# Performance work log

Measured on AMD Instinct MI355X. Metric: run time of the kernel, lower is better.

The kernel has to match this reference:

```python
import jax, jax.numpy as jnp
import numpy as np

N_EMBD = 1024
N_HEAD = 16
B, T = 4, 2048


def setup_inputs() -> dict:
    key = jax.random.key(0)
    ks = jax.random.split(key, 4)
    s = 1.0 / np.sqrt(N_EMBD)
    return {
        "x": jax.random.normal(ks[0], (B, T, N_EMBD), dtype=jnp.float32),
        "w_attn": jax.random.normal(ks[1], (N_EMBD, 3 * N_EMBD), dtype=jnp.float32) * s,
        "b_attn": jnp.zeros((3 * N_EMBD,), dtype=jnp.float32),
        "w_proj": jax.random.normal(ks[2], (N_EMBD, N_EMBD), dtype=jnp.float32) * s,
        "b_proj": jnp.zeros((N_EMBD,), dtype=jnp.float32),
    }


def reference(x, w_attn, b_attn, w_proj, b_proj):
    Bb, Tt, C = x.shape
    H = N_HEAD
    D = C // H  # head dim
    qkv = x @ w_attn + b_attn  # [B,T,3C]
    q, k, v = jnp.split(qkv, 3, axis=2)
    # [B,H,T,D]
    q = q.reshape(Bb, Tt, H, D).transpose(0, 2, 1, 3)
    k = k.reshape(Bb, Tt, H, D).transpose(0, 2, 1, 3)
    v = v.reshape(Bb, Tt, H, D).transpose(0, 2, 1, 3)
    scale = 1.0 / np.sqrt(D).astype(np.float32)
    attn = jnp.einsum("bhqd,bhkd->bhqk", q, k) * scale
    mask = jnp.tril(jnp.ones((Tt, Tt), dtype=bool))
    attn = jnp.where(mask, attn, jnp.float32(-jnp.inf))
    probs = jax.nn.softmax(attn, axis=-1)
    out = jnp.einsum("bhqk,bhkd->bhqd", probs, v)
    out = out.transpose(0, 2, 1, 3).reshape(Bb, Tt, C)
    return out @ w_proj + b_proj
```

## Files before the change

kernel.cpp:

```cpp
#include <hip/hip_runtime.h>
#include <hip/hip_bf16.h>


typedef float f32x4 __attribute__((ext_vector_type(4)));
typedef short short8 __attribute__((ext_vector_type(8)));
typedef short short4v __attribute__((ext_vector_type(4)));

__device__ __forceinline__ short f2bf(float f) {
  union { __hip_bfloat16 h; short s; } u;
  u.h = __float2bfloat16(f);
  return u.s;
}

__device__ __forceinline__ void gl_lds16(const void* g, void* l) {
  __builtin_amdgcn_global_load_lds(
      (const __attribute__((address_space(1))) void*)g,
      (__attribute__((address_space(3))) void*)l, 16, 0, 0);
}


__global__ void cvt_f32_bf16(const float* __restrict__ in, short* __restrict__ out) {
  int i = (blockIdx.x * 256 + threadIdx.x) * 4;
  float4 v = *(const float4*)(in + i);
  short4v o;
  o[0] = f2bf(v.x); o[1] = f2bf(v.y); o[2] = f2bf(v.z); o[3] = f2bf(v.w);
  *(short4v*)(out + i) = o;
}

__global__ void transpose_cvt(const float* __restrict__ in, short* __restrict__ out,
                              int K, int N) {
  __shared__ float tile[32][33];
  int bx = blockIdx.x * 32;
  int by = blockIdx.y * 32;
  int tx = threadIdx.x, ty = threadIdx.y;
#pragma unroll
  for (int i = 0; i < 32; i += 8)
    tile[ty + i][tx] = in[(size_t)(by + ty + i) * N + bx + tx];
  __syncthreads();
#pragma unroll
  for (int i = 0; i < 32; i += 8)
    out[(size_t)(bx + ty + i) * K + by + tx] = f2bf(tile[tx][ty + i]);
}


#define GEMM_BODY(A_, Bt_)                                                        \
  __shared__ __align__(16) short As[128 * 32];                                    \
  __shared__ __align__(16) short Bs[128 * 32];                                    \
  const int tid = threadIdx.x;                                                    \
  const int wv = tid >> 6;                                                        \
  const int wr = wv >> 1, wc = wv & 1;                                            \
  const int ln = tid & 15, quad = (tid & 63) >> 4;                                \
  const int m0 = blockIdx.y * 128, n0 = blockIdx.x * 128;                         \
  f32x4 acc[4][4];                                                                \
  _Pragma("unroll") for (int i = 0; i < 4; ++i)                                   \
      _Pragma("unroll") for (int j = 0; j < 4; ++j)                               \
          acc[i][j] = (f32x4){0.f, 0.f, 0.f, 0.f};                                \
  for (int k0 = 0; k0 < 1024; k0 += 32) {                                         \
    _Pragma("unroll") for (int i = 0; i < 2; ++i) {                               \
      int cc = tid + i * 256;                                                     \
      int row = cc >> 2, part = cc & 3;                                           \
      gl_lds16(A_ + (size_t)(m0 + row) * 1024 + k0 + part * 8,                    \
               (char*)As + (wv * 64 + i * 256) * 16);                             \
      gl_lds16(Bt_ + (size_t)(n0 + row) * 1024 + k0 + part * 8,                   \
               (char*)Bs + (wv * 64 + i * 256) * 16);                             \
    }                                                                             \
    __syncthreads();                                                              \
    short8 af[4], bf[4];                                                          \
    _Pragma("unroll") for (int i = 0; i < 4; ++i)                                 \
        af[i] = *(const short8*)&As[(wr * 64 + i * 16 + ln) * 32 + quad * 8];     \
    _Pragma("unroll") for (int j = 0; j < 4; ++j)                                 \
        bf[j] = *(const short8*)&Bs[(wc * 64 + j * 16 + ln) * 32 + quad * 8];     \
    _Pragma("unroll") for (int i = 0; i < 4; ++i)                                 \
        _Pragma("unroll") for (int j = 0; j < 4; ++j)                             \
            acc[i][j] =                                                           \
                __builtin_amdgcn_mfma_f32_16x16x32_bf16(af[i], bf[j], acc[i][j],  \
                                                        0, 0, 0);                 \
    __syncthreads();                                                              \
  }

__global__ __launch_bounds__(256, 2) void gemm_qkv(
    const short* __restrict__ A, const short* __restrict__ Bt,
    const float* __restrict__ bias, short* __restrict__ Qb,
    short* __restrict__ Kb, short* __restrict__ Vtb) {
  GEMM_BODY(A, Bt)
#pragma unroll
  for (int i = 0; i < 4; ++i) {
#pragma unroll
    for (int j = 0; j < 4; ++j) {
      int n = n0 + wc * 64 + j * 16 + ln;
      int n2 = n & 1023;
      int hh = n2 >> 6, d = n2 & 63;
      float bv = bias[n];
#pragma unroll
      for (int r = 0; r < 4; ++r) {
        int m = m0 + wr * 64 + i * 16 + quad * 4 + r;
        int bb = m >> 11, t = m & 2047;
        float o = acc[i][j][r] + bv;
        int bh = (bb << 4) + hh;
        if (n < 1024)
          Qb[((size_t)bh * 2048 + t) * 64 + d] = f2bf(o * 0.18033688f);
        else if (n < 2048)
          Kb[((size_t)bh * 2048 + t) * 64 + d] = f2bf(o);
        else
          Vtb[((size_t)bh * 64 + d) * 2048 + t] = f2bf(o);
      }
    }
  }
}

__global__ __launch_bounds__(256, 2) void gemm_proj(
    const short* __restrict__ A, const short* __restrict__ Bt,
    const float* __restrict__ bias, float* __restrict__ out) {
  GEMM_BODY(A, Bt)
#pragma unroll
  for (int i = 0; i < 4; ++i) {
#pragma unroll
    for (int j = 0; j < 4; ++j) {
      int n = n0 + wc * 64 + j * 16 + ln;
      float bv = bias[n];
#pragma unroll
      for (int r = 0; r < 4; ++r) {
        int m = m0 + wr * 64 + i * 16 + quad * 4 + r;
        out[(size_t)m * 1024 + n] = acc[i][j][r] + bv;
      }
    }
  }
}

__global__ __launch_bounds__(256, 3) void flash_attn(
    const short* __restrict__ Qg_, const short* __restrict__ Kg_,
    const short* __restrict__ Vg_, short* __restrict__ Ob) {
  constexpr int STR = 72;
  __shared__ __align__(16) short Kl[64 * STR];
  __shared__ __align__(16) short Vl[64 * STR];
  const int tid = threadIdx.x;
  const int wv = tid >> 6, ln = tid & 15, quad = (tid & 63) >> 4;
  const int q0 = (gridDim.x - 1 - blockIdx.x) * 128;
  const int bh = blockIdx.y;
  const short* Qg = Qg_ + (size_t)bh * 2048 * 64;
  const short* Kg = Kg_ + (size_t)bh * 2048 * 64;
  const short* Vg = Vg_ + (size_t)bh * 64 * 2048;
  const int qbase = q0 + wv * 32;

  short8 qf[2][2];
#pragma unroll
  for (int h = 0; h < 2; ++h)
#pragma unroll
    for (int ch = 0; ch < 2; ++ch)
      qf[h][ch] = *(const short8*)(Qg + (size_t)(qbase + h * 16 + ln) * 64 +
                                   ch * 32 + quad * 8);

  f32x4 Oacc[2][4];
#pragma unroll
  for (int h = 0; h < 2; ++h)
#pragma unroll
    for (int mt = 0; mt < 4; ++mt) Oacc[h][mt] = (f32x4){0.f, 0.f, 0.f, 0.f};
  float lpart[2] = {0.f, 0.f};

  const int ktmax = (q0 + 127) >> 6;
  short8 kreg[2], vreg[2];
  const int srow = tid >> 3, spart = tid & 7;

#define LOADKV(KT)                                                              \
  {                                                                             \
    const short* Kt = Kg + (size_t)(KT) * 64 * 64;                              \
    _Pragma("unroll") for (int i = 0; i < 2; ++i) {                             \
      kreg[i] = *(const short8*)(Kt + (size_t)(srow + i * 32) * 64 + spart * 8);\
      vreg[i] = *(const short8*)(Vg + (size_t)(srow + i * 32) * 2048 +          \
                                 (KT) * 64 + spart * 8);                        \
    }                                                                           \
  }

  LOADKV(0)
  for (int kt = 0; kt <= ktmax; ++kt) {
    __syncthreads();
#pragma unroll
    for (int i = 0; i < 2; ++i) {
      *(short8*)&Kl[(srow + i * 32) * STR + spart * 8] = kreg[i];
      *(short8*)&Vl[(srow + i * 32) * STR + spart * 8] = vreg[i];
    }
    __syncthreads();
    if (kt < ktmax) LOADKV(kt + 1)

    if (kt * 64 <= qbase + 31) {
      f32x4 St[2][4];
#pragma unroll
      for (int h = 0; h < 2; ++h)
#pragma unroll
        for (int kb = 0; kb < 4; ++kb) St[h][kb] = (f32x4){0.f, 0.f, 0.f, 0.f};
#pragma unroll
      for (int kb = 0; kb < 4; ++kb) {
        short8 ka0 = *(const short8*)&Kl[(kb * 16 + ln) * STR + quad * 8];
        short8 ka1 = *(const short8*)&Kl[(kb * 16 + ln) * STR + 32 + quad * 8];
#pragma unroll
        for (int h = 0; h < 2; ++h) {
          St[h][kb] = __builtin_amdgcn_mfma_f32_16x16x32_bf16(ka0, qf[h][0],
                                                              St[h][kb], 0, 0, 0);
          St[h][kb] = __builtin_amdgcn_mfma_f32_16x16x32_bf16(ka1, qf[h][1],
                                                              St[h][kb], 0, 0, 0);
        }
      }

      short4v pf[2][4];
#pragma unroll
      for (int h = 0; h < 2; ++h) {
        const bool needmask = kt * 64 + 63 > qbase + h * 16;
        const int qg = qbase + h * 16 + ln;
#pragma unroll
        for (int kb = 0; kb < 4; ++kb)
#pragma unroll
          for (int r = 0; r < 4; ++r) {
            float s = St[h][kb][r];
            if (needmask) {
              int key = kt * 64 + kb * 16 + quad * 4 + r;
              s = (key <= qg) ? s : -1e30f;
            }
            float p = __builtin_amdgcn_exp2f(s);
            lpart[h] += p;
            union { float f; unsigned u; } c;
            c.f = p;
            pf[h][kb][r] = (short)((c.u + 0x8000u) >> 16);
          }
      }

#pragma unroll
      for (int kb = 0; kb < 4; ++kb)
#pragma unroll
        for (int mt = 0; mt < 4; ++mt) {
          short4v va =
              *(const short4v*)&Vl[(mt * 16 + ln) * STR + kb * 16 + quad * 4];
#pragma unroll
          for (int h = 0; h < 2; ++h)
            Oacc[h][mt] = __builtin_amdgcn_mfma_f32_16x16x16bf16_1k(
                va, pf[h][kb], Oacc[h][mt], 0, 0, 0);
        }
    }
  }

  const int bb = bh >> 4, hh = bh & 15;
#pragma unroll
  for (int h = 0; h < 2; ++h) {
    float l = lpart[h];
    l += __shfl_xor(l, 16);
    l += __shfl_xor(l, 32);
    float rl = 1.0f / l;
    int t = qbase + h * 16 + ln;
#pragma unroll
    for (int mt = 0; mt < 4; ++mt) {
      short4v o;
#pragma unroll
      for (int r = 0; r < 4; ++r) o[r] = f2bf(Oacc[h][mt][r] * rl);
      *(short4v*)(Ob + ((size_t)(bb * 2048 + t)) * 1024 + hh * 64 + mt * 16 +
                  quad * 4) = o;
    }
  }
}


extern "C" void kernel_launch(void* const* d_in, const int* in_sizes, int n_in,
                              void* d_out, int out_size, void* d_ws, size_t ws_size,
                              hipStream_t stream) {
  const float* x      = (const float*)d_in[0];
  const float* w_attn = (const float*)d_in[1];
  const float* b_attn = (const float*)d_in[2];
  const float* w_proj = (const float*)d_in[3];
  const float* b_proj = (const float*)d_in[4];
  float* out = (float*)d_out;
  char* ws = (char*)d_ws;

  short* xb  = (short*)(ws);
  short* wat = (short*)(ws + 16777216);
  short* wpt = (short*)(ws + 23068672);
  short* Qb  = (short*)(ws + 25165824);
  short* Kb  = (short*)(ws + 41943040);
  short* Vtb = (short*)(ws + 58720256);
  short* Ob  = (short*)(ws + 75497472);

  cvt_f32_bf16<<<8192, 256, 0, stream>>>(x, xb);
  transpose_cvt<<<dim3(96, 32), dim3(32, 8), 0, stream>>>(w_attn, wat, 1024, 3072);
  transpose_cvt<<<dim3(32, 32), dim3(32, 8), 0, stream>>>(w_proj, wpt, 1024, 1024);
  gemm_qkv<<<dim3(24, 64), 256, 0, stream>>>(xb, wat, b_attn, Qb, Kb, Vtb);
  flash_attn<<<dim3(16, 64), 256, 0, stream>>>(Qb, Kb, Vtb, Ob);
  gemm_proj<<<dim3(8, 64), 256, 0, stream>>>(Ob, wpt, b_proj, out);
}
```

Measured before the change: 315.4 us.

## Double-buffer K/V in flash attention, pair causal tiles per block, transpose V separately

Flash attention now uses double-buffered LDS for K/V tiles, so each iteration needs one barrier instead of two. Each block handles a complementary pair of query tiles (long and short) to balance causal work across 512 blocks. The QKV GEMM writes V in row layout, which should make its stores coalesced, and a separate transpose kernel builds V^T, reusing the O buffer as scratch. The cost is an extra kernel launch plus a V round-trip through memory, and occupancy drops from 3 to 2 blocks per CU because of the larger LDS footprint.

```diff
diff --git a/kernel.cpp b/kernel.cpp
--- a/kernel.cpp
+++ b/kernel.cpp
@@ -40,6 +40,22 @@
 #pragma unroll
   for (int i = 0; i < 32; i += 8)
     out[(size_t)(bx + ty + i) * K + by + tx] = f2bf(tile[tx][ty + i]);
+}
+
+__global__ void transpose_v(const short* __restrict__ in, short* __restrict__ out) {
+  __shared__ short tile[32][33];
+  const int bh = blockIdx.z;
+  const int d0 = blockIdx.x * 32, t0 = blockIdx.y * 32;
+  const short* src = in + (size_t)bh * 2048 * 64;
+  short* dst = out + (size_t)bh * 64 * 2048;
+  int tx = threadIdx.x, ty = threadIdx.y;
+#pragma unroll
+  for (int i = 0; i < 4; ++i)
+    tile[ty + i * 8][tx] = src[(size_t)(t0 + ty + i * 8) * 64 + d0 + tx];
+  __syncthreads();
+#pragma unroll
+  for (int i = 0; i < 4; ++i)
+    dst[(size_t)(d0 + ty + i * 8) * 2048 + t0 + tx] = tile[tx][ty + i * 8];
 }
 
 
@@ -81,7 +97,7 @@
 __global__ __launch_bounds__(256, 2) void gemm_qkv(
     const short* __restrict__ A, const short* __restrict__ Bt,
     const float* __restrict__ bias, short* __restrict__ Qb,
-    short* __restrict__ Kb, short* __restrict__ Vtb) {
+    short* __restrict__ Kb, short* __restrict__ Vb) {
   GEMM_BODY(A, Bt)
 #pragma unroll
   for (int i = 0; i < 4; ++i) {
@@ -96,13 +112,13 @@
         int m = m0 + wr * 64 + i * 16 + quad * 4 + r;
         int bb = m >> 11, t = m & 2047;
         float o = acc[i][j][r] + bv;
-        int bh = (bb << 4) + hh;
+        size_t idx = ((size_t)((bb << 4) + hh) * 2048 + t) * 64 + d;
         if (n < 1024)
-          Qb[((size_t)bh * 2048 + t) * 64 + d] = f2bf(o * 0.18033688f);
+          Qb[idx] = f2bf(o * 0.18033688f);
         else if (n < 2048)
-          Kb[((size_t)bh * 2048 + t) * 64 + d] = f2bf(o);
+          Kb[idx] = f2bf(o);
         else
-          Vtb[((size_t)bh * 64 + d) * 2048 + t] = f2bf(o);
+          Vb[idx] = f2bf(o);
       }
     }
   }
@@ -127,39 +143,23 @@
   }
 }
 
-__global__ __launch_bounds__(256, 3) void flash_attn(
+__global__ __launch_bounds__(256, 2) void flash_attn(
     const short* __restrict__ Qg_, const short* __restrict__ Kg_,
     const short* __restrict__ Vg_, short* __restrict__ Ob) {
   constexpr int STR = 72;
-  __shared__ __align__(16) short Kl[64 * STR];
-  __shared__ __align__(16) short Vl[64 * STR];
+  __shared__ __align__(16) short Kl[2][64 * STR];
+  __shared__ __align__(16) short Vl[2][64 * STR];
   const int tid = threadIdx.x;
   const int wv = tid >> 6, ln = tid & 15, quad = (tid & 63) >> 4;
-  const int q0 = (gridDim.x - 1 - blockIdx.x) * 128;
-  const int bh = blockIdx.y;
+  const int bh = blockIdx.x & 63;
+  const int pair = blockIdx.x >> 6;
   const short* Qg = Qg_ + (size_t)bh * 2048 * 64;
   const short* Kg = Kg_ + (size_t)bh * 2048 * 64;
   const short* Vg = Vg_ + (size_t)bh * 64 * 2048;
-  const int qbase = q0 + wv * 32;
-
-  short8 qf[2][2];
-#pragma unroll
-  for (int h = 0; h < 2; ++h)
-#pragma unroll
-    for (int ch = 0; ch < 2; ++ch)
-      qf[h][ch] = *(const short8*)(Qg + (size_t)(qbase + h * 16 + ln) * 64 +
-                                   ch * 32 + quad * 8);
-
-  f32x4 Oacc[2][4];
-#pragma unroll
-  for (int h = 0; h < 2; ++h)
-#pragma unroll
-    for (int mt = 0; mt < 4; ++mt) Oacc[h][mt] = (f32x4){0.f, 0.f, 0.f, 0.f};
-  float lpart[2] = {0.f, 0.f};
-
-  const int ktmax = (q0 + 127) >> 6;
+  const int srow = tid >> 3, spart = tid & 7;
+  const int bb = bh >> 4, hh = bh & 15;
+
   short8 kreg[2], vreg[2];
-  const int srow = tid >> 3, spart = tid & 7;
 
 #define LOADKV(KT)                                                              \
   {                                                                             \
@@ -170,90 +170,127 @@
                                  (KT) * 64 + spart * 8);                        \
     }                                                                           \
   }
-
-  LOADKV(0)
-  for (int kt = 0; kt <= ktmax; ++kt) {
+#define WRITEKV(BUF)                                                            \
+  _Pragma("unroll") for (int i = 0; i < 2; ++i) {                               \
+    *(short8*)&Kl[BUF][(srow + i * 32) * STR + spart * 8] = kreg[i];            \
+    *(short8*)&Vl[BUF][(srow + i * 32) * STR + spart * 8] = vreg[i];            \
+  }
+
+#pragma unroll
+  for (int it = 0; it < 2; ++it) {
+    const int qt = it ? pair : (15 - pair);
+    const int q0 = qt * 128;
+    const int qbase = q0 + wv * 32;
+    const int nkt = (q0 >> 6) + 2;
+
+    short8 qf[2][2];
+#pragma unroll
+    for (int h = 0; h < 2; ++h)
+#pragma unroll
+      for (int ch = 0; ch < 2; ++ch)
+        qf[h][ch] = *(const short8*)(Qg + (size_t)(qbase + h * 16 + ln) * 64 +
+                                     ch * 32 + quad * 8);
+
+    f32x4 Oacc[2][4];
+#pragma unroll
+    for (int h = 0; h < 2; ++h)
+#pragma unroll
+      for (int mt = 0; mt < 4; ++mt) Oacc[h][mt] = (f32x4){0.f, 0.f, 0.f, 0.f};
+    float lpart[2] = {0.f, 0.f};
+
+    LOADKV(0)
     __syncthreads();
-#pragma unroll
-    for (int i = 0; i < 2; ++i) {
-      *(short8*)&Kl[(srow + i * 32) * STR + spart * 8] = kreg[i];
-      *(short8*)&Vl[(srow + i * 32) * STR + spart * 8] = vreg[i];
+    WRITEKV(0)
+    LOADKV(1)
+
+    for (int kt = 0; kt < nkt; ++kt) {
+      __syncthreads();
+      const short* Kcur = Kl[kt & 1];
+      const short* Vcur = Vl[kt & 1];
+      if (kt + 1 < nkt) {
+        WRITEKV((kt + 1) & 1)
+        if (kt + 2 < nkt) LOADKV(kt + 2)
+      }
+
+      if (kt * 64 <= qbase + 31) {
+        f32x4 St[2][4];
+#pragma unroll
+        for (int h = 0; h < 2; ++h)
+#pragma unroll
+          for (int kb = 0; kb < 4; ++kb) St[h][kb] = (f32x4){0.f, 0.f, 0.f, 0.f};
+#pragma unroll
+        for (int kb = 0; kb < 4; ++kb) {
+          short8 ka0 = *(const short8*)&Kcur[(kb * 16 + ln) * STR + quad * 8];
+          short8 ka1 = *(const short8*)&Kcur[(kb * 16 + ln) * STR + 32 + quad * 8];
+#pragma unroll
+          for (int h = 0; h < 2; ++h) {
+            St[h][kb] = __builtin_amdgcn_mfma_f32_16x16x32_bf16(
+                ka0, qf[h][0], St[h][kb], 0, 0, 0);
+            St[h][kb] = __builtin_amdgcn_mfma_f32_16x16x32_bf16(
+                ka1, qf[h][1], St[h][kb], 0, 0, 0);
+          }
+        }
+
+        short4v pf[2][4];
+#pragma unroll
+        for (int h = 0; h < 2; ++h) {
+          const bool needmask = kt * 64 + 63 > qbase + h * 16;
+          const int qg = qbase + h * 16 + ln;
+#pragma unroll
+          for (int kb = 0; kb < 4; ++kb) {
+            float p[4];
+#pragma unroll
+            for (int r = 0; r < 4; ++r) {
+              float s = St[h][kb][r];
+              if (needmask) {
+                int key = kt * 64 + kb * 16 + quad * 4 + r;
+                s = (key <= qg) ? s : -1e30f;
+              }
+              p[r] = __builtin_amdgcn_exp2f(s);
+              lpart[h] += p[r];
+            }
+            union { __hip_bfloat162 b2; unsigned u; } w0, w1;
+            w0.b2 = __float22bfloat162_rn(make_float2(p[0], p[1]));
+            w1.b2 = __float22bfloat162_rn(make_float2(p[2], p[3]));
+            union { short4v s4; unsigned u2[2]; } m;
+            m.u2[0] = w0.u; m.u2[1] = w1.u;
+            pf[h][kb] = m.s4;
+          }
+        }
+
+#pragma unroll
+        for (int kb = 0; kb < 4; ++kb)
+#pragma unroll
+          for (int mt = 0; mt < 4; ++mt) {
+            short4v va =
+                *(const short4v*)&Vcur[(mt * 16 + ln) * STR + kb * 16 + quad * 4];
+#pragma unroll
+            for (int h = 0; h < 2; ++h)
+              Oacc[h][mt] = __builtin_amdgcn_mfma_f32_16x16x16bf16_1k(
+                  va, pf[h][kb], Oacc[h][mt], 0, 0, 0);
+          }
+      }
     }
-    __syncthreads();
-    if (kt < ktmax) LOADKV(kt + 1)
-
-    if (kt * 64 <= qbase + 31) {
-      f32x4 St[2][4];
-#pragma unroll
-      for (int h = 0; h < 2; ++h)
-#pragma unroll
-        for (int kb = 0; kb < 4; ++kb) St[h][kb] = (f32x4){0.f, 0.f, 0.f, 0.f};
-#pragma unroll
-      for (int kb = 0; kb < 4; ++kb) {
-        short8 ka0 = *(const short8*)&Kl[(kb * 16 + ln) * STR + quad * 8];
-        short8 ka1 = *(const short8*)&Kl[(kb * 16 + ln) * STR + 32 + quad * 8];
-#pragma unroll
-        for (int h = 0; h < 2; ++h) {
-          St[h][kb] = __builtin_amdgcn_mfma_f32_16x16x32_bf16(ka0, qf[h][0],
-                                                              St[h][kb], 0, 0, 0);
-          St[h][kb] = __builtin_amdgcn_mfma_f32_16x16x32_bf16(ka1, qf[h][1],
-                                                              St[h][kb], 0, 0, 0);
-        }
-      }
-
-      short4v pf[2][4];
-#pragma unroll
-      for (int h = 0; h < 2; ++h) {
-        const bool needmask = kt * 64 + 63 > qbase + h * 16;
-        const int qg = qbase + h * 16 + ln;
-#pragma unroll
-        for (int kb = 0; kb < 4; ++kb)
-#pragma unroll
-          for (int r = 0; r < 4; ++r) {
-            float s = St[h][kb][r];
-            if (needmask) {
-              int key = kt * 64 + kb * 16 + quad * 4 + r;
-              s = (key <= qg) ? s : -1e30f;
-            }
-            float p = __builtin_amdgcn_exp2f(s);
-            lpart[h] += p;
-            union { float f; unsigned u; } c;
-            c.f = p;
-            pf[h][kb][r] = (short)((c.u + 0x8000u) >> 16);
-          }
-      }
-
-#pragma unroll
-      for (int kb = 0; kb < 4; ++kb)
-#pragma unroll
-        for (int mt = 0; mt < 4; ++mt) {
-          short4v va =
-              *(const short4v*)&Vl[(mt * 16 + ln) * STR + kb * 16 + quad * 4];
-#pragma unroll
-          for (int h = 0; h < 2; ++h)
-            Oacc[h][mt] = __builtin_amdgcn_mfma_f32_16x16x16bf16_1k(
-                va, pf[h][kb], Oacc[h][mt], 0, 0, 0);
-        }
+
+#pragma unroll
+    for (int h = 0; h < 2; ++h) {
+      float l = lpart[h];
+      l += __shfl_xor(l, 16);
+      l += __shfl_xor(l, 32);
+      float rl = 1.0f / l;
+      int t = qbase + h * 16 + ln;
+#pragma unroll
+      for (int mt = 0; mt < 4; ++mt) {
+        short4v o;
+#pragma unroll
+        for (int r = 0; r < 4; ++r) o[r] = f2bf(Oacc[h][mt][r] * rl);
+        *(short4v*)(Ob + ((size_t)(bb * 2048 + t)) * 1024 + hh * 64 + mt * 16 +
+                    quad * 4) = o;
+      }
     }
   }
-
-  const int bb = bh >> 4, hh = bh & 15;
-#pragma unroll
-  for (int h = 0; h < 2; ++h) {
-    float l = lpart[h];
-    l += __shfl_xor(l, 16);
-    l += __shfl_xor(l, 32);
-    float rl = 1.0f / l;
-    int t = qbase + h * 16 + ln;
-#pragma unroll
-    for (int mt = 0; mt < 4; ++mt) {
-      short4v o;
-#pragma unroll
-      for (int r = 0; r < 4; ++r) o[r] = f2bf(Oacc[h][mt][r] * rl);
-      *(short4v*)(Ob + ((size_t)(bb * 2048 + t)) * 1024 + hh * 64 + mt * 16 +
-                  quad * 4) = o;
-    }
-  }
+#undef LOADKV
+#undef WRITEKV
 }
 
 
@@ -275,11 +312,13 @@
   short* Kb  = (short*)(ws + 41943040);
   short* Vtb = (short*)(ws + 58720256);
   short* Ob  = (short*)(ws + 75497472);
+  short* Vb  = Ob;
 
   cvt_f32_bf16<<<8192, 256, 0, stream>>>(x, xb);
   transpose_cvt<<<dim3(96, 32), dim3(32, 8), 0, stream>>>(w_attn, wat, 1024, 3072);
   transpose_cvt<<<dim3(32, 32), dim3(32, 8), 0, stream>>>(w_proj, wpt, 1024, 1024);
-  gemm_qkv<<<dim3(24, 64), 256, 0, stream>>>(xb, wat, b_attn, Qb, Kb, Vtb);
-  flash_attn<<<dim3(16, 64), 256, 0, stream>>>(Qb, Kb, Vtb, Ob);
+  gemm_qkv<<<dim3(24, 64), 256, 0, stream>>>(xb, wat, b_attn, Qb, Kb, Vb);
+  transpose_v<<<dim3(2, 64, 64), dim3(32, 8), 0, stream>>>(Vb, Vtb);
+  flash_attn<<<512, 256, 0, stream>>>(Qb, Kb, Vtb, Ob);
   gemm_proj<<<dim3(8, 64), 256, 0, stream>>>(Ob, wpt, b_proj, out);
 }
```

New measurement: 269.9 us. -14.4%, faster.
